# Performance work log

Measured on AMD Instinct MI355X. Metric: run time of the kernel, lower is better.

The kernel has to match this reference:

```python
import jax, jax.numpy as jnp
import numpy as np

B, N, DIM, H, DH, K = 4, 2048, 512, 6, 64, 16
KEEP_PROB = 0.9  # 1 - dropout_rate
LOG2PI = float(np.log(2.0 * np.pi))
LOG_PRIOR = float(np.log(1.0 / K))


def setup_inputs() -> dict:
    key = jax.random.key(0)
    ks = jax.random.split(key, 7)
    inputs_q = jax.random.normal(ks[0], (B, N, DIM), dtype=jnp.float32)
    # decoder-style causal mask, shape [B, 1, q_len, kv_len]
    causal = jnp.tril(jnp.ones((N, N), dtype=jnp.float32))
    mask = jnp.broadcast_to(causal[None, None], (B, 1, N, N))
    # dropout keep mask broadcast across the query dim: [B, H, 1, kv_len]
    keep = jax.random.bernoulli(ks[1], KEEP_PROB, (B, H, 1, N)).astype(jnp.float32)
    w_qkv = jax.random.normal(ks[2], (DIM, 3 * H * DH), dtype=jnp.float32) * 0.02
    w_out = jax.random.normal(ks[3], (H * DH, DIM), dtype=jnp.float32) * 0.02
    mu_lookup = jax.random.normal(ks[4], (K, DIM), dtype=jnp.float32)
    logvar_lookup = jax.random.normal(ks[5], (K, DIM), dtype=jnp.float32) * 0.1
    return {
        "inputs_q": inputs_q,
        "mask": mask,
        "keep": keep,
        "w_qkv": w_qkv,
        "w_out": w_out,
        "mu_lookup": mu_lookup,
        "logvar_lookup": logvar_lookup,
    }


def reference(inputs_q, mask, keep, w_qkv, w_out, mu_lookup, logvar_lookup):
    # --- MultiHeadDotProductAttention (self-attn path) ---
    qkv = (inputs_q @ w_qkv).reshape(B, N, 3, H, DH)  # [B,N,3,H,DH]
    q, k, v = qkv[:, :, 0], qkv[:, :, 1], qkv[:, :, 2]
    # bias: 0 where mask > 0, -1e10 elsewhere (note: no 1/sqrt(d) scaling, as in source)
    bias = jnp.where(mask > 0, 0.0, -1e10)
    attn_weights = jnp.einsum('bqhd,bkhd->bhqk', q, k) + bias  # [B,H,N,N]
    attn_weights = jax.nn.softmax(attn_weights, axis=-1)
    # broadcast dropout: mask shared across the query dim
    attn_weights = attn_weights * keep / KEEP_PROB
    attn_out = jnp.einsum('bhqk,bkhd->bqhd', attn_weights, v)
    attn_out = attn_out.reshape(B, N, H * DH) @ w_out  # [B,N,DIM]

    # --- GMM posterior approx q(y|x) ~= p(y|z) (approx_qy_x, vectorized over k) ---
    z = attn_out.mean(axis=1)  # pooled latent, [B,DIM]
    diff = z[:, None, :] - mu_lookup[None]  # [B,K,DIM]
    llh = -0.5 * jnp.sum(
        diff * diff / jnp.exp(logvar_lookup)[None] + logvar_lookup[None] + LOG2PI,
        axis=-1,
    )  # [B,K]
    logLogit_qy_x = llh + LOG_PRIOR
    qy_x = jax.nn.softmax(logLogit_qy_x, axis=1)  # [B,K]

    # combine mixture mean back in so both branches are live in one output
    return attn_out + (qy_x @ mu_lookup)[:, None, :]
```

## Files before the change

### kernel.cpp

```cpp
#include <hip/hip_runtime.h>
#include <cstdint>
#include <cstddef>

#define NH 6
#define NSEQ 2048
#define DIMD 512
#define BATCH 4
#define HD 384
#define LOG2PI_F 1.8378770664093453f

typedef __attribute__((ext_vector_type(8))) short short8;
typedef __attribute__((ext_vector_type(8))) unsigned short ushort8;
typedef __attribute__((ext_vector_type(4))) unsigned short ushort4v;
typedef __attribute__((ext_vector_type(4))) float floatx4;

__device__ inline unsigned short f2bf(float f){
  unsigned int u = __float_as_uint(f);
  u += 0x7FFFu + ((u>>16)&1u);
  return (unsigned short)(u>>16);
}

#define GLD16(gp, lp) __builtin_amdgcn_global_load_lds( \
  (const __attribute__((address_space(1))) void*)(gp), \
  (__attribute__((address_space(3))) void*)(lp), 16, 0, 0)

__global__ __launch_bounds__(256) void convert_x(
    const float* __restrict__ xq, unsigned short* __restrict__ xbf)
{
  int i = blockIdx.x*256 + threadIdx.x;
  floatx4 v = *(const floatx4*)(xq + (size_t)i*4);
  ushort4v r;
  #pragma unroll
  for(int j=0;j<4;j++) r[j] = f2bf(v[j]);
  *(ushort4v*)(xbf + (size_t)i*4) = r;
}

__global__ __launch_bounds__(256) void wtrans(
    const float* __restrict__ src, unsigned short* __restrict__ dst, int R, int C)
{
  __shared__ __attribute__((aligned(16))) unsigned short Ls[64*72];
  const int t = threadIdx.x;
  const int r = t>>2, c0 = (t&3)*16;
  const int d0 = blockIdx.y*64, n0 = blockIdx.x*64;
  #pragma unroll
  for (int j=0;j<16;j+=4){
    floatx4 v = *(const floatx4*)(src + (size_t)(d0+r)*C + n0 + c0 + j);
    #pragma unroll
    for(int jj=0;jj<4;jj++) Ls[r*72 + c0+j+jj] = f2bf(v[jj]);
  }
  __syncthreads();
  #pragma unroll
  for (int j=0;j<16;j+=8){
    ushort8 o;
    #pragma unroll
    for(int jj=0;jj<8;jj++) o[jj] = Ls[(c0+j+jj)*72 + r];
    *(ushort8*)(dst + (size_t)(n0+r)*R + d0 + c0 + j) = o;
  }
}

__global__ __launch_bounds__(256) void gemm_qkv(
    const unsigned short* __restrict__ A,
    const unsigned short* __restrict__ Bt,
    const float* __restrict__ keep,
    unsigned short* __restrict__ Qo, unsigned short* __restrict__ Ko, unsigned short* __restrict__ Vt)
{
  __shared__ __attribute__((aligned(16))) unsigned short As[128*64];
  __shared__ __attribute__((aligned(16))) unsigned short Bs[128*64];
  const int tid = threadIdx.x;
  const int w = tid>>6, lane = tid&63;
  const int wr = w>>1, wc = w&1;
  const int quad = lane>>4, l16 = lane&15;
  const int tM = blockIdx.y*128, tN = blockIdx.x*128;
  const int r8 = lane>>3, c8 = (lane&7)*8;
  floatx4 acc[4][4];
  floatx4 zed = {0.f,0.f,0.f,0.f};
  #pragma unroll
  for (int i=0;i<4;i++)
    #pragma unroll
    for(int j=0;j<4;j++) acc[i][j] = zed;

  for (int k0=0; k0<512; k0+=64){
    #pragma unroll
    for (int i=0;i<4;i++){
      int row = w*32 + i*8;
      GLD16(A  + (size_t)(tM+row+r8)*512 + k0 + c8, As + row*64);
      GLD16(Bt + (size_t)(tN+row+r8)*512 + k0 + c8, Bs + row*64);
    }
    __syncthreads();
    #pragma unroll
    for (int kk=0; kk<64; kk+=32){
      short8 af[4], bf[4];
      #pragma unroll
      for(int mt=0;mt<4;mt++)
        af[mt] = *(const short8*)(As + (wr*64+mt*16+l16)*64 + kk + quad*8);
      #pragma unroll
      for(int nt=0;nt<4;nt++)
        bf[nt] = *(const short8*)(Bs + (wc*64+nt*16+l16)*64 + kk + quad*8);
      #pragma unroll
      for(int mt=0;mt<4;mt++)
        #pragma unroll
        for(int nt=0;nt<4;nt++)
          acc[mt][nt] = __builtin_amdgcn_mfma_f32_16x16x32_bf16(af[mt], bf[nt], acc[mt][nt], 0,0,0);
    }
    __syncthreads();
  }
  #pragma unroll
  for(int nt=0;nt<4;nt++){
    int gcol = tN + wc*64 + nt*16 + l16;
    int t = gcol/384;
    int rem = gcol - t*384;
    int h = rem>>6, dh = rem&63;
    #pragma unroll
    for(int mt=0;mt<4;mt++){
      int grow = tM + wr*64 + mt*16 + quad*4;
      #pragma unroll
      for(int r=0;r<4;r++){
        int row = grow + r;
        int b = row>>11, n = row & 2047;
        if (t==0)      Qo[(size_t)((b*NH + h)*NSEQ + n)*64 + dh] = f2bf(acc[mt][nt][r]);
        else if (t==1) Ko[(size_t)((b*NH + h)*NSEQ + n)*64 + dh] = f2bf(acc[mt][nt][r]);
        else {
          float kp = keep[(size_t)(b*NH + h)*NSEQ + n];
          Vt[(size_t)((b*NH + h)*64 + dh)*NSEQ + n] = f2bf(acc[mt][nt][r]*kp);
        }
      }
    }
  }
}

__global__ __launch_bounds__(256,3) void attn_kernel(
    const unsigned short* __restrict__ Qg, const unsigned short* __restrict__ Kg,
    const unsigned short* __restrict__ VtG,
    unsigned short* __restrict__ atp)
{
  __shared__ __attribute__((aligned(16))) unsigned short Ks[64*64];
  __shared__ __attribute__((aligned(16))) unsigned short Vs[64*64];
  __shared__ __attribute__((aligned(16))) unsigned short Ps[4*32*72];
  const int tid = threadIdx.x;
  const int w = tid>>6, lane = tid&63;
  const int quad = lane>>4, l16 = lane&15;
  const int bx = 15 - (int)blockIdx.x;
  const int bh = blockIdx.y;
  const int b = bh/NH, h = bh - b*NH;
  const unsigned short* Qb = Qg  + (size_t)bh*NSEQ*64;
  const unsigned short* Kb = Kg  + (size_t)bh*NSEQ*64;
  const unsigned short* Vb = VtG + (size_t)bh*64*NSEQ;
  const int q0 = bx*128 + w*32;
  const int nkt_w  = 2*bx + 1 + (w>>1);
  const int nkt_max= 2*bx + 2;
  const int gr = lane>>3, gc = (lane&7)*8;

  short8 qf[2][2];
  #pragma unroll
  for(int mt=0;mt<2;mt++)
    #pragma unroll
    for(int kc=0;kc<2;kc++)
      qf[mt][kc] = *(const short8*)(Qb + (size_t)(q0+mt*16+l16)*64 + kc*32 + quad*8);

  short8 onesf;
  #pragma unroll
  for(int j=0;j<8;j++) onesf[j] = (short)0x3F80;

  floatx4 O[2][4];
  floatx4 accl[2];
  floatx4 zed = {0.f,0.f,0.f,0.f};
  #pragma unroll
  for(int mt=0;mt<2;mt++){
    #pragma unroll
    for(int dt=0;dt<4;dt++) O[mt][dt] = zed;
    accl[mt] = zed;
  }
  unsigned short* Pw = Ps + w*2304;

  for (int kt=0; kt<nkt_max; kt++){
    const int kB = kt*64;
    #pragma unroll
    for(int ro=0; ro<2; ro++){
      int r0 = ro*32 + w*8;
      GLD16(Kb + (size_t)(kB + r0 + gr)*64 + gc, Ks + r0*64);
      GLD16(Vb + (size_t)(r0 + gr)*NSEQ + kB + gc, Vs + r0*64);
    }
    __syncthreads();
    if (kt < nkt_w){
      short8 kf[4][2];
      #pragma unroll
      for(int nt=0;nt<4;nt++)
        #pragma unroll
        for(int kc=0;kc<2;kc++)
          kf[nt][kc] = *(const short8*)(Ks + (nt*16+l16)*64 + kc*32 + quad*8);

      floatx4 sacc[2][4];
      floatx4 m12 = {-12.f,-12.f,-12.f,-12.f};
      #pragma unroll
      for(int mt=0;mt<2;mt++)
        #pragma unroll
        for(int nt=0;nt<4;nt++) sacc[mt][nt] = m12;
      #pragma unroll
      for(int mt=0;mt<2;mt++)
        #pragma unroll
        for(int nt=0;nt<4;nt++)
          #pragma unroll
          for(int kc=0;kc<2;kc++)
            sacc[mt][nt] = __builtin_amdgcn_mfma_f32_16x16x32_bf16(qf[mt][kc], kf[nt][kc], sacc[mt][nt], 0,0,0);

      const bool dia = (kt == nkt_w-1);
      #pragma unroll
      for(int mt=0;mt<2;mt++){
        #pragma unroll
        for(int nt=0;nt<4;nt++){
          int key = kB + nt*16 + l16;
          #pragma unroll
          for(int r=0;r<4;r++){
            float p = __expf(sacc[mt][nt][r]);
            if (dia) p = (key <= q0 + mt*16 + quad*4 + r) ? p : 0.f;
            Pw[(mt*16+quad*4+r)*72 + nt*16 + l16] = f2bf(p);
          }
        }
      }
      short8 vf[2][4];
      #pragma unroll
      for(int kh=0;kh<2;kh++)
        #pragma unroll
        for(int dt=0;dt<4;dt++)
          vf[kh][dt] = *(const short8*)(Vs + (dt*16+l16)*64 + kh*32 + quad*8);
      #pragma unroll
      for(int kh=0;kh<2;kh++){
        #pragma unroll
        for(int mt=0;mt<2;mt++){
          short8 pf = *(const short8*)(Pw + (mt*16+l16)*72 + kh*32 + quad*8);
          accl[mt] = __builtin_amdgcn_mfma_f32_16x16x32_bf16(pf, onesf, accl[mt], 0,0,0);
          #pragma unroll
          for(int dt=0;dt<4;dt++)
            O[mt][dt] = __builtin_amdgcn_mfma_f32_16x16x32_bf16(pf, vf[kh][dt], O[mt][dt], 0,0,0);
        }
      }
    }
    __syncthreads();
  }

  #pragma unroll
  for(int mt=0;mt<2;mt++){
    #pragma unroll
    for(int r=0;r<4;r++){
      int q = q0 + mt*16 + quad*4 + r;
      float sc = (1.0f/0.9f) / accl[mt][r];
      #pragma unroll
      for(int dt=0;dt<4;dt++)
        atp[((size_t)(b*NSEQ + q))*HD + h*64 + dt*16 + l16] = f2bf(O[mt][dt][r]*sc);
    }
  }
}

__global__ __launch_bounds__(256) void gemm_proj(
    const unsigned short* __restrict__ A,
    const unsigned short* __restrict__ Bt,
    float* __restrict__ Co,
    float* __restrict__ z)
{
  __shared__ __attribute__((aligned(16))) unsigned short As[128*64];
  __shared__ __attribute__((aligned(16))) unsigned short Bs[128*64];
  const int tid = threadIdx.x;
  const int w = tid>>6, lane = tid&63;
  const int wr = w>>1, wc = w&1;
  const int quad = lane>>4, l16 = lane&15;
  const int tM = blockIdx.y*128, tN = blockIdx.x*128;
  const int r8 = lane>>3, c8 = (lane&7)*8;
  floatx4 acc[4][4];
  floatx4 zed = {0.f,0.f,0.f,0.f};
  #pragma unroll
  for (int i=0;i<4;i++)
    #pragma unroll
    for(int j=0;j<4;j++) acc[i][j] = zed;

  for (int k0=0; k0<384; k0+=64){
    #pragma unroll
    for (int i=0;i<4;i++){
      int row = w*32 + i*8;
      GLD16(A  + (size_t)(tM+row+r8)*384 + k0 + c8, As + row*64);
      GLD16(Bt + (size_t)(tN+row+r8)*384 + k0 + c8, Bs + row*64);
    }
    __syncthreads();
    #pragma unroll
    for (int kk=0; kk<64; kk+=32){
      short8 af[4], bf[4];
      #pragma unroll
      for(int mt=0;mt<4;mt++)
        af[mt] = *(const short8*)(As + (wr*64+mt*16+l16)*64 + kk + quad*8);
      #pragma unroll
      for(int nt=0;nt<4;nt++)
        bf[nt] = *(const short8*)(Bs + (wc*64+nt*16+l16)*64 + kk + quad*8);
      #pragma unroll
      for(int mt=0;mt<4;mt++)
        #pragma unroll
        for(int nt=0;nt<4;nt++)
          acc[mt][nt] = __builtin_amdgcn_mfma_f32_16x16x32_bf16(af[mt], bf[nt], acc[mt][nt], 0,0,0);
    }
    __syncthreads();
  }
  #pragma unroll
  for(int mt=0;mt<4;mt++){
    int grow = tM + wr*64 + mt*16 + quad*4;
    #pragma unroll
    for(int nt=0;nt<4;nt++){
      int gcol = tN + wc*64 + nt*16 + l16;
      #pragma unroll
      for(int r=0;r<4;r++)
        Co[(size_t)(grow+r)*512 + gcol] = acc[mt][nt][r];
    }
  }
  #pragma unroll
  for(int nt=0;nt<4;nt++){
    float s = 0.f;
    #pragma unroll
    for(int mt=0;mt<4;mt++)
      #pragma unroll
      for(int r=0;r<4;r++) s += acc[mt][nt][r];
    s += __shfl_xor(s, 16, 64);
    s += __shfl_xor(s, 32, 64);
    if (quad == 0){
      int gcol = tN + wc*64 + nt*16 + l16;
      atomicAdd(&z[(tM>>11)*DIMD + gcol], s);
    }
  }
}

__global__ __launch_bounds__(256) void gmm_kernel(
    const float* __restrict__ z, const float* __restrict__ mu,
    const float* __restrict__ lv, float* __restrict__ c)
{
  __shared__ float sh[16];
  __shared__ float qy[16];
  int tid = threadIdx.x;
  int k = tid>>4, li = tid&15;
  int b = blockIdx.x;
  float part = 0.f;
  for(int d=li; d<DIMD; d+=16){
    float zz = z[b*DIMD+d] * (1.0f/2048.0f);
    float m = mu[k*DIMD+d], l = lv[k*DIMD+d];
    float diff = zz - m;
    part += diff*diff*__expf(-l) + l + LOG2PI_F;
  }
  #pragma unroll
  for(int off=8;off>=1;off>>=1) part += __shfl_xor(part, off, 64);
  if (li==0) sh[k] = part;
  __syncthreads();
  if (tid<16){
    float logit = -0.5f*sh[tid];
    float mx = logit;
    #pragma unroll
    for(int off=8;off>=1;off>>=1) mx = fmaxf(mx, __shfl_xor(mx, off, 64));
    float e = __expf(logit-mx);
    float se = e;
    #pragma unroll
    for(int off=8;off>=1;off>>=1) se += __shfl_xor(se, off, 64);
    qy[tid] = e/se;
  }
  __syncthreads();
  for(int d=tid; d<DIMD; d+=256){
    float accv = 0.f;
    #pragma unroll
    for(int kk=0;kk<16;kk++) accv += qy[kk]*mu[kk*DIMD+d];
    c[b*DIMD+d] = accv;
  }
}

__global__ __launch_bounds__(256) void final_add(
    const float* __restrict__ ao, const float* __restrict__ c, float* __restrict__ out)
{
  size_t i = ((size_t)blockIdx.x*256 + threadIdx.x)*4;
  int d = (int)(i & 511);
  int b = (int)(i >> 20);
  floatx4 a = *(const floatx4*)(ao + i);
  floatx4 cc = *(const floatx4*)(c + b*DIMD + d);
  *(floatx4*)(out + i) = a + cc;
}

extern "C" void kernel_launch(void* const* d_in, const int* in_sizes, int n_in,
                              void* d_out, int out_size, void* d_ws, size_t ws_size,
                              hipStream_t stream) {
  const float* inputs_q = (const float*)d_in[0];
  const float* keep  = (const float*)d_in[2];
  const float* w_qkv = (const float*)d_in[3];
  const float* w_out = (const float*)d_in[4];
  const float* mu    = (const float*)d_in[5];
  const float* lv    = (const float*)d_in[6];
  float* out = (float*)d_out;
  char* ws = (char*)d_ws;
  size_t off = 0;
  auto alloc = [&](size_t bytes){ void* p = ws + off; off += (bytes + 255) & ~(size_t)255; return p; };
  unsigned short* Qb  = (unsigned short*)alloc((size_t)24*2048*64*2);
  unsigned short* Kb  = (unsigned short*)alloc((size_t)24*2048*64*2);
  unsigned short* Vt  = (unsigned short*)alloc((size_t)24*64*2048*2);
  unsigned short* xbf = (unsigned short*)alloc((size_t)8192*512*2);
  unsigned short* wqT = (unsigned short*)alloc((size_t)1152*512*2);
  unsigned short* woT = (unsigned short*)alloc((size_t)512*384*2);
  unsigned short* atp = (unsigned short*)alloc((size_t)8192*384*2);
  float* ao = (float*)alloc((size_t)8192*512*4);
  float* z  = (float*)alloc((size_t)4*512*4);
  float* c  = (float*)alloc((size_t)4*512*4);

  hipMemsetAsync(z, 0, 4*512*4, stream);
  convert_x<<<4096, 256, 0, stream>>>(inputs_q, xbf);
  wtrans<<<dim3(18,8), 256, 0, stream>>>(w_qkv, wqT, 512, 1152);
  wtrans<<<dim3(8,6),  256, 0, stream>>>(w_out, woT, 384, 512);
  gemm_qkv<<<dim3(9,64), 256, 0, stream>>>(xbf, wqT, keep, Qb, Kb, Vt);
  attn_kernel<<<dim3(16,24), 256, 0, stream>>>(Qb, Kb, Vt, atp);
  gemm_proj<<<dim3(4,64), 256, 0, stream>>>(atp, woT, ao, z);
  gmm_kernel<<<4, 256, 0, stream>>>(z, mu, lv, c);
  final_add<<<4096, 256, 0, stream>>>(ao, c, out);
}
```

Baseline: 265.8 us.

## Double-buffer K/V tiles, swizzle LDS layout, and rebalance attention grid to 64-row blocks

The attention kernel now uses 128-thread blocks covering 64 query rows each, with a 1D grid of 768 blocks ordered so the longest causal rows run first and heads are interleaved. K/V tiles are double-buffered, so the next tile's global-to-LDS load is issued while the current tile is computed, leaving one barrier per iteration. An XOR swizzle on the LDS column layout is meant to cut bank conflicts on fragment reads. In exchange the kernel uses more LDS per block and drops the occupancy hint.

```diff
diff --git a/kernel.cpp b/kernel.cpp
--- a/kernel.cpp
+++ b/kernel.cpp
@@ -128,27 +128,30 @@
   }
 }
 
-__global__ __launch_bounds__(256,3) void attn_kernel(
+__global__ __launch_bounds__(128) void attn_kernel(
     const unsigned short* __restrict__ Qg, const unsigned short* __restrict__ Kg,
     const unsigned short* __restrict__ VtG,
     unsigned short* __restrict__ atp)
 {
-  __shared__ __attribute__((aligned(16))) unsigned short Ks[64*64];
-  __shared__ __attribute__((aligned(16))) unsigned short Vs[64*64];
-  __shared__ __attribute__((aligned(16))) unsigned short Ps[4*32*72];
+  __shared__ __attribute__((aligned(16))) unsigned short Ks[2][64*64];
+  __shared__ __attribute__((aligned(16))) unsigned short Vs[2][64*64];
+  __shared__ __attribute__((aligned(16))) unsigned short Ps[2*32*72];
   const int tid = threadIdx.x;
   const int w = tid>>6, lane = tid&63;
   const int quad = lane>>4, l16 = lane&15;
-  const int bx = 15 - (int)blockIdx.x;
-  const int bh = blockIdx.y;
+  const int bid = blockIdx.x;
+  const int t3  = bid>>3;
+  const int bh  = (bid&7) + 8*(t3 % 3);
+  const int c   = 31 - (t3/3);
   const int b = bh/NH, h = bh - b*NH;
   const unsigned short* Qb = Qg  + (size_t)bh*NSEQ*64;
   const unsigned short* Kb = Kg  + (size_t)bh*NSEQ*64;
   const unsigned short* Vb = VtG + (size_t)bh*64*NSEQ;
-  const int q0 = bx*128 + w*32;
-  const int nkt_w  = 2*bx + 1 + (w>>1);
-  const int nkt_max= 2*bx + 2;
-  const int gr = lane>>3, gc = (lane&7)*8;
+  const int q0 = c*64 + w*32;
+  const int nkt = c + 1;
+  const int gr = lane>>3;
+  const int sc = (((lane&7) ^ gr))*8;
+  const int sw = (l16&7);
 
   short8 qf[2][2];
   #pragma unroll
@@ -172,70 +175,79 @@
   }
   unsigned short* Pw = Ps + w*2304;
 
-  for (int kt=0; kt<nkt_max; kt++){
+  auto stage = [&](int kt, int bb){
     const int kB = kt*64;
-    #pragma unroll
-    for(int ro=0; ro<2; ro++){
-      int r0 = ro*32 + w*8;
-      GLD16(Kb + (size_t)(kB + r0 + gr)*64 + gc, Ks + r0*64);
-      GLD16(Vb + (size_t)(r0 + gr)*NSEQ + kB + gc, Vs + r0*64);
-    }
+    unsigned short* Kd = Ks[bb];
+    unsigned short* Vd = Vs[bb];
+    #pragma unroll
+    for(int i=0;i<4;i++){
+      int r0 = i*16 + w*8;
+      GLD16(Kb + (size_t)(kB + r0 + gr)*64 + sc, Kd + r0*64);
+      GLD16(Vb + (size_t)(r0 + gr)*NSEQ + kB + sc, Vd + r0*64);
+    }
+  };
+
+  stage(0, 0);
+  for (int kt=0; kt<nkt; kt++){
+    const int cur = kt&1;
     __syncthreads();
-    if (kt < nkt_w){
-      short8 kf[4][2];
+    if (kt+1 < nkt) stage(kt+1, cur^1);
+    const unsigned short* Kd = Ks[cur];
+    const unsigned short* Vd = Vs[cur];
+    const int kB = kt*64;
+
+    short8 kf[4][2];
+    #pragma unroll
+    for(int nt=0;nt<4;nt++)
+      #pragma unroll
+      for(int kc=0;kc<2;kc++)
+        kf[nt][kc] = *(const short8*)(Kd + (nt*16+l16)*64 + (((kc*4+quad) ^ sw)<<3));
+
+    floatx4 sacc[2][4];
+    floatx4 m12 = {-12.f,-12.f,-12.f,-12.f};
+    #pragma unroll
+    for(int mt=0;mt<2;mt++)
+      #pragma unroll
+      for(int nt=0;nt<4;nt++) sacc[mt][nt] = m12;
+    #pragma unroll
+    for(int mt=0;mt<2;mt++)
       #pragma unroll
       for(int nt=0;nt<4;nt++)
         #pragma unroll
         for(int kc=0;kc<2;kc++)
-          kf[nt][kc] = *(const short8*)(Ks + (nt*16+l16)*64 + kc*32 + quad*8);
-
-      floatx4 sacc[2][4];
-      floatx4 m12 = {-12.f,-12.f,-12.f,-12.f};
-      #pragma unroll
-      for(int mt=0;mt<2;mt++)
+          sacc[mt][nt] = __builtin_amdgcn_mfma_f32_16x16x32_bf16(qf[mt][kc], kf[nt][kc], sacc[mt][nt], 0,0,0);
+
+    const bool dia = (kt == nkt-1);
+    #pragma unroll
+    for(int mt=0;mt<2;mt++){
+      #pragma unroll
+      for(int nt=0;nt<4;nt++){
+        int key = kB + nt*16 + l16;
         #pragma unroll
-        for(int nt=0;nt<4;nt++) sacc[mt][nt] = m12;
-      #pragma unroll
-      for(int mt=0;mt<2;mt++)
-        #pragma unroll
-        for(int nt=0;nt<4;nt++)
-          #pragma unroll
-          for(int kc=0;kc<2;kc++)
-            sacc[mt][nt] = __builtin_amdgcn_mfma_f32_16x16x32_bf16(qf[mt][kc], kf[nt][kc], sacc[mt][nt], 0,0,0);
-
-      const bool dia = (kt == nkt_w-1);
-      #pragma unroll
-      for(int mt=0;mt<2;mt++){
-        #pragma unroll
-        for(int nt=0;nt<4;nt++){
-          int key = kB + nt*16 + l16;
-          #pragma unroll
-          for(int r=0;r<4;r++){
-            float p = __expf(sacc[mt][nt][r]);
-            if (dia) p = (key <= q0 + mt*16 + quad*4 + r) ? p : 0.f;
-            Pw[(mt*16+quad*4+r)*72 + nt*16 + l16] = f2bf(p);
-          }
+        for(int r=0;r<4;r++){
+          float p = __expf(sacc[mt][nt][r]);
+          if (dia) p = (key <= q0 + mt*16 + quad*4 + r) ? p : 0.f;
+          Pw[(mt*16+quad*4+r)*72 + nt*16 + l16] = f2bf(p);
         }
       }
-      short8 vf[2][4];
-      #pragma unroll
-      for(int kh=0;kh<2;kh++)
+    }
+    short8 vf[2][4];
+    #pragma unroll
+    for(int kh=0;kh<2;kh++)
+      #pragma unroll
+      for(int dt=0;dt<4;dt++)
+        vf[kh][dt] = *(const short8*)(Vd + (dt*16+l16)*64 + (((kh*4+quad) ^ sw)<<3));
+    #pragma unroll
+    for(int kh=0;kh<2;kh++){
+      #pragma unroll
+      for(int mt=0;mt<2;mt++){
+        short8 pf = *(const short8*)(Pw + (mt*16+l16)*72 + kh*32 + quad*8);
+        accl[mt] = __builtin_amdgcn_mfma_f32_16x16x32_bf16(pf, onesf, accl[mt], 0,0,0);
         #pragma unroll
         for(int dt=0;dt<4;dt++)
-          vf[kh][dt] = *(const short8*)(Vs + (dt*16+l16)*64 + kh*32 + quad*8);
-      #pragma unroll
-      for(int kh=0;kh<2;kh++){
-        #pragma unroll
-        for(int mt=0;mt<2;mt++){
-          short8 pf = *(const short8*)(Pw + (mt*16+l16)*72 + kh*32 + quad*8);
-          accl[mt] = __builtin_amdgcn_mfma_f32_16x16x32_bf16(pf, onesf, accl[mt], 0,0,0);
-          #pragma unroll
-          for(int dt=0;dt<4;dt++)
-            O[mt][dt] = __builtin_amdgcn_mfma_f32_16x16x32_bf16(pf, vf[kh][dt], O[mt][dt], 0,0,0);
-        }
+          O[mt][dt] = __builtin_amdgcn_mfma_f32_16x16x32_bf16(pf, vf[kh][dt], O[mt][dt], 0,0,0);
       }
     }
-    __syncthreads();
   }
 
   #pragma unroll
@@ -243,10 +255,10 @@
     #pragma unroll
     for(int r=0;r<4;r++){
       int q = q0 + mt*16 + quad*4 + r;
-      float sc = (1.0f/0.9f) / accl[mt][r];
+      float sc2 = (1.0f/0.9f) / accl[mt][r];
       #pragma unroll
       for(int dt=0;dt<4;dt++)
-        atp[((size_t)(b*NSEQ + q))*HD + h*64 + dt*16 + l16] = f2bf(O[mt][dt][r]*sc);
+        atp[((size_t)(b*NSEQ + q))*HD + h*64 + dt*16 + l16] = f2bf(O[mt][dt][r]*sc2);
     }
   }
 }
@@ -404,7 +416,7 @@
   wtrans<<<dim3(18,8), 256, 0, stream>>>(w_qkv, wqT, 512, 1152);
   wtrans<<<dim3(8,6),  256, 0, stream>>>(w_out, woT, 384, 512);
   gemm_qkv<<<dim3(9,64), 256, 0, stream>>>(xbf, wqT, keep, Qb, Kb, Vt);
-  attn_kernel<<<dim3(16,24), 256, 0, stream>>>(Qb, Kb, Vt, atp);
+  attn_kernel<<<768, 128, 0, stream>>>(Qb, Kb, Vt, atp);
   gemm_proj<<<dim3(4,64), 256, 0, stream>>>(atp, woT, ao, z);
   gmm_kernel<<<4, 256, 0, stream>>>(z, mu, lv, c);
   final_add<<<4096, 256, 0, stream>>>(ao, c, out);
```

New measurement: 247.8 us. 1.07x faster.
